# Performance work log

Hardware: AMD Instinct MI355X
Metric: run time of the kernel (lower is better)

## Reference

```python
import jax, jax.numpy as jnp
import numpy as np

B, N, DIM = 1, 512, 1024
HEADS, DH = 16, 64          # dim_head = 64, _dim = heads*dh = 1024
P = 32                      # projection_dim
P2 = P // 2
NEG_INF = -1e30


def setup_inputs() -> dict:
    key = jax.random.key(0)
    ks = jax.random.split(key, 14)
    s = 0.02
    _dim = HEADS * DH
    return {
        "x":    jax.random.normal(ks[0], (B, N, DIM), dtype=jnp.float32),
        "Wqkv": jax.random.normal(ks[1], (3 * _dim, DIM), dtype=jnp.float32) * s,
        "Wout": jax.random.normal(ks[2], (DIM, _dim), dtype=jnp.float32) * s,
        "Wq":   jax.random.normal(ks[3], (P, DH), dtype=jnp.float32) * s,
        "bq":   jax.random.normal(ks[4], (P,), dtype=jnp.float32) * s,
        "Wk":   jax.random.normal(ks[5], (P, DH), dtype=jnp.float32) * s,
        "bk":   jax.random.normal(ks[6], (P,), dtype=jnp.float32) * s,
        "W1":   jax.random.normal(ks[7], (P, 2 * P), dtype=jnp.float32) * s,
        "b1":   jax.random.normal(ks[8], (P,), dtype=jnp.float32) * s,
        "W2":   jax.random.normal(ks[9], (P2, P), dtype=jnp.float32) * s,
        "b2":   jax.random.normal(ks[10], (P2,), dtype=jnp.float32) * s,
        "W3":   jax.random.normal(ks[11], (1, P2), dtype=jnp.float32) * s,
        "b3":   jax.random.normal(ks[12], (1,), dtype=jnp.float32) * s,
    }


def reference(x, Wqkv, Wout, Wq, bq, Wk, bk, W1, b1, W2, b2, W3, b3):
    b, n, _ = x.shape
    # qkv projection, then einops 'b n (d k h) -> k b h n d' split (d outermost!)
    qkv = jnp.einsum('bnc,oc->bno', x, Wqkv).reshape(b, n, DH, 3, HEADS)
    q = jnp.transpose(qkv[:, :, :, 0, :], (0, 3, 1, 2))  # [b,h,n,dh]
    k = jnp.transpose(qkv[:, :, :, 1, :], (0, 3, 1, 2))
    v = jnp.transpose(qkv[:, :, :, 2, :], (0, 3, 1, 2))

    qp = jnp.einsum('bhnd,pd->bhnp', q, Wq) + bq  # [b,h,n,P]
    kp = jnp.einsum('bhnd,pd->bhnp', k, Wk) + bk

    # linear1 on concat(q_i, k_j): split W1 -> broadcast-add (same math,
    # avoids materializing the [b,h,n,n,2P] concat tensor)
    W1q, W1k = W1[:, :P], W1[:, P:]
    a = jnp.einsum('bhnp,qp->bhnq', qp, W1q)      # [b,h,n,P]
    c = jnp.einsum('bhnp,qp->bhnq', kp, W1k)      # [b,h,n,P]
    h1 = jax.nn.relu(a[:, :, :, None, :] + c[:, :, None, :, :] + b1)  # [b,h,n,n,P]
    h2 = jax.nn.relu(jnp.einsum('bhijp,qp->bhijq', h1, W2) + b2)      # [b,h,n,n,P/2]
    score = jnp.einsum('bhijq,oq->bhijo', h2, W3)[..., 0] + b3[0]     # [b,h,n,n]

    # causal mask (triu(1) filled with -inf)
    i = jnp.arange(n)
    causal = i[None, :] > i[:, None]
    score = jnp.where(causal, NEG_INF, score)

    attn = jax.nn.softmax(score, axis=-1)
    out = jnp.einsum('bhij,bhjd->bhid', attn, v)                      # [b,h,n,dh]
    out = jnp.transpose(out, (0, 2, 1, 3)).reshape(b, n, HEADS * DH)  # b n (h d)
    return jnp.einsum('bne,oe->bno', out, Wout)
```

## Files before the change

### kernel.cpp

```cpp
#include <hip/hip_runtime.h>
#include <hip/hip_bf16.h>
#include <hip/hip_fp16.h>
#include <math.h>

#define N_SEQ 512
#define DIM   1024
#define HEADS 16
#define DH    64
#define P     32
#define P2    16

typedef short    bf16x8 __attribute__((ext_vector_type(8)));
typedef _Float16 f16x8  __attribute__((ext_vector_type(8)));
typedef float    f32x4  __attribute__((ext_vector_type(4)));

__device__ inline unsigned short f2bf(float f) {
  union { float f; unsigned u; } v; v.f = f;
  unsigned r = (v.u + 0x7fffu + ((v.u >> 16) & 1u)) >> 16;
  return (unsigned short)r;
}

union H8 { f16x8 v; __half2 h2[4]; unsigned u32[4]; };

__global__ __launch_bounds__(256) void prep(
    const float* __restrict__ Wqkv, const float* __restrict__ Wq,
    const float* __restrict__ bq, const float* __restrict__ Wk,
    const float* __restrict__ bk, const float* __restrict__ W1,
    const float* __restrict__ x, const float* __restrict__ Wout,
    short* __restrict__ Wcomb, short* __restrict__ xb,
    short* __restrict__ Woutb, float* __restrict__ ba32,
    float* __restrict__ bc32) {
  const int b = blockIdx.x, tid = threadIdx.x;
  if (b < 256) {
    __shared__ float W1s[32][33];
    __shared__ float Wqs[32][65];
    __shared__ float wsm[32][65];
    __shared__ __align__(16) float qs[64][132];
    const int part = b >> 7, rem = b & 127;
    const int h = rem >> 3, c0 = (rem & 7) * 128;
    const int grow = part * 16 + h;
    for (int idx = tid; idx < 1024; idx += 256)
      W1s[idx >> 5][idx & 31] = W1[(idx >> 5) * 64 + part * 32 + (idx & 31)];
    const float* Wsel = part ? Wk : Wq;
    for (int idx = tid; idx < 2048; idx += 256)
      Wqs[idx >> 6][idx & 63] = Wsel[idx];
    for (int idx = tid; idx < 2048; idx += 256) {
      const int d = idx >> 5, c4 = idx & 31;
      *(float4*)&qs[d][c4 * 4] =
          *(const float4*)(Wqkv + (size_t)(d * 48 + grow) * DIM + c0 + c4 * 4);
    }
    __syncthreads();
    for (int idx = tid; idx < 2048; idx += 256) {
      const int q = idx >> 6, d = idx & 63;
      float s = 0.f;
#pragma unroll
      for (int p = 0; p < 32; ++p) s += W1s[q][p] * Wqs[p][d];
      wsm[q][d] = s;
    }
    __syncthreads();
    for (int idx = tid; idx < 4096; idx += 256) {
      const int q = idx >> 7, c = idx & 127;
      float s = 0.f;
#pragma unroll
      for (int d = 0; d < 64; ++d) s += wsm[q][d] * qs[d][c];
      Wcomb[(size_t)(part * 512 + h * 32 + q) * DIM + c0 + c] = (short)f2bf(s);
    }
    if (rem == 0 && tid < 32) {
      const float* bsel = part ? bk : bq;
      float s = 0.f;
#pragma unroll
      for (int p = 0; p < 32; ++p) s += W1s[tid][p] * bsel[p];
      (part ? bc32 : ba32)[tid] = s;
    }
  } else if (b < 384) {
#pragma unroll
    for (int rr = 0; rr < 8; ++rr) {
      const int ov = (b - 256) * 8 + rr;
      const int h = ov >> 6, d = ov & 63;
      const float4 v = *(const float4*)(Wqkv + (size_t)(d * 48 + 32 + h) * DIM + tid * 4);
      ushort4 o;
      o.x = f2bf(v.x); o.y = f2bf(v.y); o.z = f2bf(v.z); o.w = f2bf(v.w);
      *(ushort4*)(Wcomb + (size_t)(1024 + ov) * DIM + tid * 4) = o;
    }
  } else if (b < 512) {
    const int idx = (b - 384) * 256 + tid;
#pragma unroll
    for (int u = 0; u < 4; ++u) {
      const int t = u * 32768 + idx;
      const float4 v = ((const float4*)x)[t];
      ushort4 o;
      o.x = f2bf(v.x); o.y = f2bf(v.y); o.z = f2bf(v.z); o.w = f2bf(v.w);
      ((ushort4*)xb)[t] = o;
    }
  } else {
    const int idx = (b - 512) * 256 + tid;
#pragma unroll
    for (int u = 0; u < 4; ++u) {
      const int t = u * 65536 + idx;
      const float4 v = ((const float4*)Wout)[t];
      ushort4 o;
      o.x = f2bf(v.x); o.y = f2bf(v.y); o.z = f2bf(v.z); o.w = f2bf(v.w);
      ((ushort4*)Woutb)[t] = o;
    }
  }
}

__global__ __launch_bounds__(256) void gemm_acv(
    const short* __restrict__ xb, const short* __restrict__ Wcomb,
    const float* __restrict__ ba32, const float* __restrict__ bc32,
    const float* __restrict__ b1,
    __half* __restrict__ a_buf, __half* __restrict__ cb_buf,
    __half* __restrict__ vT) {
  const int wave = blockIdx.x * 4 + (threadIdx.x >> 6);
  const int tm = wave >> 6;
  const int tn = wave & 63;
  const int lane = threadIdx.x & 63;
  const int m = lane & 15;
  const int quad = lane >> 4;

  const short* pa  = xb + (size_t)(tm * 16 + m) * DIM + quad * 8;
  const short* pb0 = Wcomb + (size_t)(tn * 32 + m) * DIM + quad * 8;
  const short* pb1 = pb0 + (size_t)16 * DIM;

  f32x4 acc0 = {0.f,0.f,0.f,0.f}, acc1 = {0.f,0.f,0.f,0.f};
#pragma unroll 4
  for (int k = 0; k < DIM; k += 32) {
    const bf16x8 av = *(const bf16x8*)(pa + k);
    const bf16x8 b0 = *(const bf16x8*)(pb0 + k);
    const bf16x8 b1v = *(const bf16x8*)(pb1 + k);
    acc0 = __builtin_amdgcn_mfma_f32_16x16x32_bf16(av, b0, acc0, 0, 0, 0);
    acc1 = __builtin_amdgcn_mfma_f32_16x16x32_bf16(av, b1v, acc1, 0, 0, 0);
  }

#pragma unroll
  for (int r = 0; r < 4; ++r) {
    const int n = tm * 16 + quad * 4 + r;
#pragma unroll
    for (int half = 0; half < 2; ++half) {
      const int o = tn * 32 + m + half * 16;
      const float val = half ? acc1[r] : acc0[r];
      if (o < 512) {
        const int h = o >> 5, q = o & 31;
        a_buf[((size_t)h * N_SEQ + n) * P + q] = __float2half(val + ba32[q]);
      } else if (o < 1024) {
        const int oo = o - 512, h = oo >> 5, q = oo & 31;
        cb_buf[((size_t)h * N_SEQ + n) * P + q] = __float2half(val + bc32[q] + b1[q]);
      } else {
        const int ov = o - 1024, h = ov >> 6, d = ov & 63;
        vT[((size_t)h * DH + d) * N_SEQ + n] = __float2half(val);
      }
    }
  }
}

__device__ inline float rowscore(const H8& a, const H8& c, f16x8 w2f,
                                 float4 b2q, float4 w3q) {
  H8 u;
#pragma unroll
  for (int k = 0; k < 4; ++k) {
    const __half2 s = __hadd2(a.h2[k], c.h2[k]);
    union { __half2 h; unsigned u; } cv; cv.h = s;
    const unsigned msk = (cv.u >> 15) & 0x00010001u;
    u.u32[k] = cv.u & ~(msk * 0xFFFFu);
  }
  f32x4 acc = {0.f, 0.f, 0.f, 0.f};
  acc = __builtin_amdgcn_mfma_f32_16x16x32_f16(w2f, u.v, acc, 0, 0, 0);
  return fmaxf(acc[0] + b2q.x, 0.f) * w3q.x + fmaxf(acc[1] + b2q.y, 0.f) * w3q.y
       + fmaxf(acc[2] + b2q.z, 0.f) * w3q.z + fmaxf(acc[3] + b2q.w, 0.f) * w3q.w;
}

__global__ __launch_bounds__(64) void attn_score(
    const __half* __restrict__ a_g, const __half* __restrict__ cb_g,
    const float* __restrict__ W2, const float* __restrict__ b2,
    const float* __restrict__ W3, const float* __restrict__ b3,
    __half* __restrict__ prob) {
  const int it = blockIdx.x;
  const int h  = blockIdx.y;
  const int lane = threadIdx.x;
  const int m = lane & 15, quad = lane >> 4;

  __shared__ __align__(16) float sc[4][528];

  const int r0 = 2 * it, r1 = 2 * it + 1;
  const int r2 = 510 - 2 * it, r3 = 511 - 2 * it;
  const int n0 = (r0 >> 4) + 1, n1 = (r1 >> 4) + 1;
  const int n2 = (r2 >> 4) + 1, n3 = (r3 >> 4) + 1;
  const int ntq = (quad == 0) ? n0 : (quad == 1) ? n1 : (quad == 2) ? n2 : n3;

  f16x8 w2f;
  {
    const float4* wp = (const float4*)(W2 + m * P + quad * 8);
    const float4 w0 = wp[0], w1 = wp[1];
    H8 u;
    u.h2[0] = __floats2half2_rn(w0.x, w0.y);
    u.h2[1] = __floats2half2_rn(w0.z, w0.w);
    u.h2[2] = __floats2half2_rn(w1.x, w1.y);
    u.h2[3] = __floats2half2_rn(w1.z, w1.w);
    w2f = u.v;
  }
  const float4 b2q = *(const float4*)(b2 + quad * 4);
  const float4 w3q = *(const float4*)(W3 + quad * 4);
  const float b3v = b3[0];

  H8 a0, a1, a2, a3;
  a0.v = *(const f16x8*)(a_g + ((size_t)h * N_SEQ + r0) * P + quad * 8);
  a1.v = *(const f16x8*)(a_g + ((size_t)h * N_SEQ + r1) * P + quad * 8);
  a2.v = *(const f16x8*)(a_g + ((size_t)h * N_SEQ + r2) * P + quad * 8);
  a3.v = *(const f16x8*)(a_g + ((size_t)h * N_SEQ + r3) * P + quad * 8);

  float p0 = 0.f, p1 = 0.f, p2 = 0.f, p3 = 0.f;
  for (int jt = 0; jt < n3; ++jt) {
    H8 cb;
    cb.v = *(const f16x8*)(cb_g + ((size_t)h * N_SEQ + jt * 16 + m) * P + quad * 8);
    p3 = rowscore(a3, cb, w2f, b2q, w3q);
    if (jt < n2) p2 = rowscore(a2, cb, w2f, b2q, w3q);
    if (jt < n1) p1 = rowscore(a1, cb, w2f, b2q, w3q);
    if (jt < n0) p0 = rowscore(a0, cb, w2f, b2q, w3q);

    const float sx = (quad & 1) ? p0 : p1;
    const float sy = (quad & 1) ? p2 : p3;
    const float rx = __shfl_xor(sx, 16);
    const float ry = __shfl_xor(sy, 16);
    const float aa = ((quad & 1) ? p1 : p0) + rx;
    const float bb = ((quad & 1) ? p3 : p2) + ry;
    const float sz = (quad & 2) ? aa : bb;
    const float rz = __shfl_xor(sz, 32);
    const float fin = ((quad & 2) ? bb : aa) + rz;

    if (jt < ntq) sc[quad][jt * 16 + m] = fin + b3v;
  }
  __syncthreads();

  const int base = lane * 8;
#pragma unroll
  for (int r = 0; r < 4; ++r) {
    const int rq = (r == 0) ? r0 : (r == 1) ? r1 : (r == 2) ? r2 : r3;
    float v[8];
    *(float4*)&v[0] = *(const float4*)&sc[r][base];
    *(float4*)&v[4] = *(const float4*)&sc[r][base + 4];
    float mx = -1e30f;
#pragma unroll
    for (int u = 0; u < 8; ++u) if (base + u <= rq) mx = fmaxf(mx, v[u]);
#pragma unroll
    for (int msk = 1; msk < 64; msk <<= 1) mx = fmaxf(mx, __shfl_xor(mx, msk));
    float e[8], sum = 0.f;
#pragma unroll
    for (int u = 0; u < 8; ++u) {
      e[u] = (base + u <= rq) ? __expf(v[u] - mx) : 0.f;
      sum += e[u];
    }
#pragma unroll
    for (int msk = 1; msk < 64; msk <<= 1) sum += __shfl_xor(sum, msk);
    const float inv = 1.f / sum;
    H8 o;
    o.h2[0] = __floats2half2_rn(e[0] * inv, e[1] * inv);
    o.h2[1] = __floats2half2_rn(e[2] * inv, e[3] * inv);
    o.h2[2] = __floats2half2_rn(e[4] * inv, e[5] * inv);
    o.h2[3] = __floats2half2_rn(e[6] * inv, e[7] * inv);
    *(f16x8*)(prob + ((size_t)h * N_SEQ + rq) * N_SEQ + base) = o.v;
  }
}

__global__ __launch_bounds__(256) void attn_pv(
    const __half* __restrict__ prob, const __half* __restrict__ vT,
    short* __restrict__ attnb) {
  const int wave = blockIdx.x * 4 + (threadIdx.x >> 6);
  const int h = wave >> 7;
  const int rem = wave & 127;
  const int tm = rem >> 2;
  const int tn = rem & 3;
  const int lane = threadIdx.x & 63;
  const int m = lane & 15, quad = lane >> 4;

  const __half* pa = prob + ((size_t)h * N_SEQ + tm * 16 + m) * N_SEQ + quad * 8;
  const __half* pb = vT + ((size_t)h * DH + tn * 16 + m) * N_SEQ + quad * 8;

  f32x4 acc = {0.f, 0.f, 0.f, 0.f};
  const int kmax = tm * 16 + 16;
  for (int k = 0; k < kmax; k += 32) {
    const f16x8 a = *(const f16x8*)(pa + k);
    const f16x8 b = *(const f16x8*)(pb + k);
    acc = __builtin_amdgcn_mfma_f32_16x16x32_f16(a, b, acc, 0, 0, 0);
  }
#pragma unroll
  for (int r = 0; r < 4; ++r)
    attnb[(size_t)(tm * 16 + quad * 4 + r) * DIM + h * DH + tn * 16 + m] =
        (short)f2bf(acc[r]);
}

__global__ __launch_bounds__(256) void gemm_out16(
    const short* __restrict__ A, const short* __restrict__ B,
    float* __restrict__ C) {
  const int wave = blockIdx.x * 4 + (threadIdx.x >> 6);
  const int tm = wave >> 6;
  const int tn = wave & 63;
  const int lane = threadIdx.x & 63;
  const int m = lane & 15, quad = lane >> 4;

  const short* pa = A + (size_t)(tm * 16 + m) * DIM + quad * 8;
  const short* pb = B + (size_t)(tn * 16 + m) * DIM + quad * 8;

  f32x4 acc = {0.f, 0.f, 0.f, 0.f};
#pragma unroll 4
  for (int k = 0; k < DIM; k += 32) {
    const bf16x8 a = *(const bf16x8*)(pa + k);
    const bf16x8 b = *(const bf16x8*)(pb + k);
    acc = __builtin_amdgcn_mfma_f32_16x16x32_bf16(a, b, acc, 0, 0, 0);
  }
#pragma unroll
  for (int r = 0; r < 4; ++r)
    C[(size_t)(tm * 16 + quad * 4 + r) * DIM + tn * 16 + m] = acc[r];
}

extern "C" void kernel_launch(void* const* d_in, const int* in_sizes, int n_in,
                              void* d_out, int out_size, void* d_ws, size_t ws_size,
                              hipStream_t stream) {
  const float* x    = (const float*)d_in[0];
  const float* Wqkv = (const float*)d_in[1];
  const float* Wout = (const float*)d_in[2];
  const float* Wq   = (const float*)d_in[3];
  const float* bq   = (const float*)d_in[4];
  const float* Wk   = (const float*)d_in[5];
  const float* bk   = (const float*)d_in[6];
  const float* W1   = (const float*)d_in[7];
  const float* b1   = (const float*)d_in[8];
  const float* W2   = (const float*)d_in[9];
  const float* b2   = (const float*)d_in[10];
  const float* W3   = (const float*)d_in[11];
  const float* b3   = (const float*)d_in[12];
  float* out = (float*)d_out;

  float*  ws     = (float*)d_ws;
  float*  ba32   = ws;
  float*  bc32   = ba32 + 32;
  __half* a_buf  = (__half*)(bc32 + 32);
  __half* cb_buf = a_buf + (size_t)HEADS * N_SEQ * P;
  __half* vT     = cb_buf + (size_t)HEADS * N_SEQ * P;
  __half* prob   = vT + (size_t)HEADS * DH * N_SEQ;
  short*  Wcomb  = (short*)(prob + (size_t)HEADS * N_SEQ * N_SEQ);
  short*  xb     = Wcomb + (size_t)2048 * DIM;
  short*  Woutb  = xb + (size_t)N_SEQ * DIM;
  short*  attnb  = Woutb + (size_t)DIM * DIM;

  prep<<<768, 256, 0, stream>>>(Wqkv, Wq, bq, Wk, bk, W1, x, Wout,
                                Wcomb, xb, Woutb, ba32, bc32);

  gemm_acv<<<512, 256, 0, stream>>>(xb, Wcomb, ba32, bc32, b1,
                                    a_buf, cb_buf, vT);

  dim3 g3(128, HEADS);
  attn_score<<<g3, 64, 0, stream>>>(a_buf, cb_buf, W2, b2, W3, b3, prob);

  attn_pv<<<512, 256, 0, stream>>>(prob, vT, attnb);

  gemm_out16<<<512, 256, 0, stream>>>(attnb, Woutb, out);
}
```

Before: 178.0 us.

## Fuse pairwise score, softmax and PV into one attention kernel

Merges the score/softmax kernel and the P·V kernel into one kernel that keeps a 32-row probability tile in shared memory as fp16. This removes the global round trip of the [16,512,512] prob matrix and one launch. It also drops b3 because softmax is shift-invariant, and applies the 1/sum normalization after the PV MFMA. The grid shrinks from 2048 single-wave blocks to 256 four-wave blocks. Raw scores stored in fp16 before softmax may reduce precision, and the lower block count may underuse the GPU.

```diff
diff --git a/kernel.cpp b/kernel.cpp
--- a/kernel.cpp
+++ b/kernel.cpp
@@ -9,6 +9,7 @@
 #define DH    64
 #define P     32
 #define P2    16
+#define PSTR  520
 
 typedef short    bf16x8 __attribute__((ext_vector_type(8)));
 typedef _Float16 f16x8  __attribute__((ext_vector_type(8)));
@@ -169,123 +170,145 @@
        + fmaxf(acc[2] + b2q.z, 0.f) * w3q.z + fmaxf(acc[3] + b2q.w, 0.f) * w3q.w;
 }
 
-__global__ __launch_bounds__(64) void attn_score(
+__device__ inline float quadreduce4(float p0, float p1, float p2, float p3,
+                                    int quad) {
+  const float sx = (quad & 1) ? p0 : p1;
+  const float sy = (quad & 1) ? p2 : p3;
+  const float rx = __shfl_xor(sx, 16);
+  const float ry = __shfl_xor(sy, 16);
+  const float aa = ((quad & 1) ? p1 : p0) + rx;
+  const float bb = ((quad & 1) ? p3 : p2) + ry;
+  const float sz = (quad & 2) ? aa : bb;
+  const float rz = __shfl_xor(sz, 32);
+  return ((quad & 2) ? bb : aa) + rz;
+}
+
+__global__ __launch_bounds__(256) void attn_fused(
     const __half* __restrict__ a_g, const __half* __restrict__ cb_g,
     const float* __restrict__ W2, const float* __restrict__ b2,
-    const float* __restrict__ W3, const float* __restrict__ b3,
-    __half* __restrict__ prob) {
-  const int it = blockIdx.x;
-  const int h  = blockIdx.y;
-  const int lane = threadIdx.x;
+    const float* __restrict__ W3,
+    const __half* __restrict__ vT, short* __restrict__ attnb) {
+  const int p = blockIdx.x;
+  const int h = blockIdx.y;
+  const int tid = threadIdx.x;
+  const int w = tid >> 6;
+  const int lane = tid & 63;
   const int m = lane & 15, quad = lane >> 4;
 
-  __shared__ __align__(16) float sc[4][528];
-
-  const int r0 = 2 * it, r1 = 2 * it + 1;
-  const int r2 = 510 - 2 * it, r3 = 511 - 2 * it;
-  const int n0 = (r0 >> 4) + 1, n1 = (r1 >> 4) + 1;
-  const int n2 = (r2 >> 4) + 1, n3 = (r3 >> 4) + 1;
-  const int ntq = (quad == 0) ? n0 : (quad == 1) ? n1 : (quad == 2) ? n2 : n3;
-
-  f16x8 w2f;
+  __shared__ __align__(16) __half probS[32][PSTR];
+  __shared__ float invS[32];
+
+  const int tlo = p, thi = 31 - p;
+  const int nlo = p + 1, nhi = 32 - p;
+
   {
-    const float4* wp = (const float4*)(W2 + m * P + quad * 8);
-    const float4 w0 = wp[0], w1 = wp[1];
-    H8 u;
-    u.h2[0] = __floats2half2_rn(w0.x, w0.y);
-    u.h2[1] = __floats2half2_rn(w0.z, w0.w);
-    u.h2[2] = __floats2half2_rn(w1.x, w1.y);
-    u.h2[3] = __floats2half2_rn(w1.z, w1.w);
-    w2f = u.v;
-  }
-  const float4 b2q = *(const float4*)(b2 + quad * 4);
-  const float4 w3q = *(const float4*)(W3 + quad * 4);
-  const float b3v = b3[0];
-
-  H8 a0, a1, a2, a3;
-  a0.v = *(const f16x8*)(a_g + ((size_t)h * N_SEQ + r0) * P + quad * 8);
-  a1.v = *(const f16x8*)(a_g + ((size_t)h * N_SEQ + r1) * P + quad * 8);
-  a2.v = *(const f16x8*)(a_g + ((size_t)h * N_SEQ + r2) * P + quad * 8);
-  a3.v = *(const f16x8*)(a_g + ((size_t)h * N_SEQ + r3) * P + quad * 8);
-
-  float p0 = 0.f, p1 = 0.f, p2 = 0.f, p3 = 0.f;
-  for (int jt = 0; jt < n3; ++jt) {
-    H8 cb;
-    cb.v = *(const f16x8*)(cb_g + ((size_t)h * N_SEQ + jt * 16 + m) * P + quad * 8);
-    p3 = rowscore(a3, cb, w2f, b2q, w3q);
-    if (jt < n2) p2 = rowscore(a2, cb, w2f, b2q, w3q);
-    if (jt < n1) p1 = rowscore(a1, cb, w2f, b2q, w3q);
-    if (jt < n0) p0 = rowscore(a0, cb, w2f, b2q, w3q);
-
-    const float sx = (quad & 1) ? p0 : p1;
-    const float sy = (quad & 1) ? p2 : p3;
-    const float rx = __shfl_xor(sx, 16);
-    const float ry = __shfl_xor(sy, 16);
-    const float aa = ((quad & 1) ? p1 : p0) + rx;
-    const float bb = ((quad & 1) ? p3 : p2) + ry;
-    const float sz = (quad & 2) ? aa : bb;
-    const float rz = __shfl_xor(sz, 32);
-    const float fin = ((quad & 2) ? bb : aa) + rz;
-
-    if (jt < ntq) sc[quad][jt * 16 + m] = fin + b3v;
+    f16x8 w2f;
+    {
+      const float4* wp = (const float4*)(W2 + m * P + quad * 8);
+      const float4 w0 = wp[0], w1 = wp[1];
+      H8 u;
+      u.h2[0] = __floats2half2_rn(w0.x, w0.y);
+      u.h2[1] = __floats2half2_rn(w0.z, w0.w);
+      u.h2[2] = __floats2half2_rn(w1.x, w1.y);
+      u.h2[3] = __floats2half2_rn(w1.z, w1.w);
+      w2f = u.v;
+    }
+    const float4 b2q = *(const float4*)(b2 + quad * 4);
+    const float4 w3q = *(const float4*)(W3 + quad * 4);
+
+    H8 alo[4], ahi[4];
+#pragma unroll
+    for (int r = 0; r < 4; ++r) {
+      alo[r].v = *(const f16x8*)(a_g + ((size_t)h * N_SEQ + tlo * 16 + 4 * w + r) * P + quad * 8);
+      ahi[r].v = *(const f16x8*)(a_g + ((size_t)h * N_SEQ + thi * 16 + 4 * w + r) * P + quad * 8);
+    }
+
+    for (int jt = 0; jt < nhi; ++jt) {
+      H8 cb;
+      cb.v = *(const f16x8*)(cb_g + ((size_t)h * N_SEQ + jt * 16 + m) * P + quad * 8);
+      const float q0 = rowscore(ahi[0], cb, w2f, b2q, w3q);
+      const float q1 = rowscore(ahi[1], cb, w2f, b2q, w3q);
+      const float q2 = rowscore(ahi[2], cb, w2f, b2q, w3q);
+      const float q3 = rowscore(ahi[3], cb, w2f, b2q, w3q);
+      const float fh = quadreduce4(q0, q1, q2, q3, quad);
+      probS[16 + 4 * w + quad][jt * 16 + m] = __float2half(fh);
+      if (jt < nlo) {
+        const float s0 = rowscore(alo[0], cb, w2f, b2q, w3q);
+        const float s1 = rowscore(alo[1], cb, w2f, b2q, w3q);
+        const float s2 = rowscore(alo[2], cb, w2f, b2q, w3q);
+        const float s3 = rowscore(alo[3], cb, w2f, b2q, w3q);
+        const float fl = quadreduce4(s0, s1, s2, s3, quad);
+        probS[4 * w + quad][jt * 16 + m] = __float2half(fl);
+      }
+    }
   }
   __syncthreads();
 
-  const int base = lane * 8;
-#pragma unroll
-  for (int r = 0; r < 4; ++r) {
-    const int rq = (r == 0) ? r0 : (r == 1) ? r1 : (r == 2) ? r2 : r3;
-    float v[8];
-    *(float4*)&v[0] = *(const float4*)&sc[r][base];
-    *(float4*)&v[4] = *(const float4*)&sc[r][base + 4];
+  {
+    const int lr = 8 * w + (lane >> 3);
+    const int c  = lane & 7;
+    const int gi = (lr < 16) ? (tlo * 16 + lr) : (thi * 16 + (lr - 16));
     float mx = -1e30f;
 #pragma unroll
-    for (int u = 0; u < 8; ++u) if (base + u <= rq) mx = fmaxf(mx, v[u]);
-#pragma unroll
-    for (int msk = 1; msk < 64; msk <<= 1) mx = fmaxf(mx, __shfl_xor(mx, msk));
-    float e[8], sum = 0.f;
-#pragma unroll
-    for (int u = 0; u < 8; ++u) {
-      e[u] = (base + u <= rq) ? __expf(v[u] - mx) : 0.f;
-      sum += e[u];
-    }
-#pragma unroll
-    for (int msk = 1; msk < 64; msk <<= 1) sum += __shfl_xor(sum, msk);
-    const float inv = 1.f / sum;
-    H8 o;
-    o.h2[0] = __floats2half2_rn(e[0] * inv, e[1] * inv);
-    o.h2[1] = __floats2half2_rn(e[2] * inv, e[3] * inv);
-    o.h2[2] = __floats2half2_rn(e[4] * inv, e[5] * inv);
-    o.h2[3] = __floats2half2_rn(e[6] * inv, e[7] * inv);
-    *(f16x8*)(prob + ((size_t)h * N_SEQ + rq) * N_SEQ + base) = o.v;
-  }
-}
-
-__global__ __launch_bounds__(256) void attn_pv(
-    const __half* __restrict__ prob, const __half* __restrict__ vT,
-    short* __restrict__ attnb) {
-  const int wave = blockIdx.x * 4 + (threadIdx.x >> 6);
-  const int h = wave >> 7;
-  const int rem = wave & 127;
-  const int tm = rem >> 2;
-  const int tn = rem & 3;
-  const int lane = threadIdx.x & 63;
-  const int m = lane & 15, quad = lane >> 4;
-
-  const __half* pa = prob + ((size_t)h * N_SEQ + tm * 16 + m) * N_SEQ + quad * 8;
-  const __half* pb = vT + ((size_t)h * DH + tn * 16 + m) * N_SEQ + quad * 8;
-
-  f32x4 acc = {0.f, 0.f, 0.f, 0.f};
-  const int kmax = tm * 16 + 16;
-  for (int k = 0; k < kmax; k += 32) {
-    const f16x8 a = *(const f16x8*)(pa + k);
-    const f16x8 b = *(const f16x8*)(pb + k);
-    acc = __builtin_amdgcn_mfma_f32_16x16x32_f16(a, b, acc, 0, 0, 0);
-  }
-#pragma unroll
-  for (int r = 0; r < 4; ++r)
-    attnb[(size_t)(tm * 16 + quad * 4 + r) * DIM + h * DH + tn * 16 + m] =
-        (short)f2bf(acc[r]);
+    for (int k = 0; k < 8; ++k) {
+      const int c0 = k * 64 + c * 8;
+      if (c0 > gi) break;
+      H8 vv; vv.v = *(const f16x8*)&probS[lr][c0];
+#pragma unroll
+      for (int u = 0; u < 8; ++u) {
+        const float s = __half2float(vv.h2[u >> 1].data[u & 1]);
+        if (c0 + u <= gi) mx = fmaxf(mx, s);
+      }
+    }
+#pragma unroll
+    for (int msk = 1; msk < 8; msk <<= 1) mx = fmaxf(mx, __shfl_xor(mx, msk));
+    float sum = 0.f;
+#pragma unroll
+    for (int k = 0; k < 8; ++k) {
+      const int c0 = k * 64 + c * 8;
+      H8 vv; vv.v = *(const f16x8*)&probS[lr][c0];
+      H8 o;
+#pragma unroll
+      for (int u = 0; u < 4; ++u) {
+        float e0 = 0.f, e1 = 0.f;
+        if (c0 + 2 * u <= gi) {
+          e0 = __expf(__half2float(vv.h2[u].data[0]) - mx);
+          if (c0 + 2 * u + 1 <= gi)
+            e1 = __expf(__half2float(vv.h2[u].data[1]) - mx);
+        }
+        sum += e0 + e1;
+        o.h2[u] = __floats2half2_rn(e0, e1);
+      }
+      *(f16x8*)&probS[lr][c0] = o.v;
+    }
+#pragma unroll
+    for (int msk = 1; msk < 8; msk <<= 1) sum += __shfl_xor(sum, msk);
+    if (c == 0) invS[lr] = 1.f / sum;
+  }
+  __syncthreads();
+
+  {
+    const int d0 = w * 16;
+    const __half* pb = vT + ((size_t)h * DH + d0 + m) * N_SEQ + quad * 8;
+#pragma unroll
+    for (int half = 0; half < 2; ++half) {
+      const int lbase = half ? 16 : 0;
+      const int tile = half ? thi : tlo;
+      const int nk = half ? ((33 - p) >> 1) : ((p + 2) >> 1);
+      f32x4 acc = {0.f, 0.f, 0.f, 0.f};
+      for (int k = 0; k < nk; ++k) {
+        const f16x8 a = *(const f16x8*)&probS[lbase + m][k * 32 + quad * 8];
+        const f16x8 b = *(const f16x8*)(pb + k * 32);
+        acc = __builtin_amdgcn_mfma_f32_16x16x32_f16(a, b, acc, 0, 0, 0);
+      }
+#pragma unroll
+      for (int r = 0; r < 4; ++r) {
+        const int lrow = quad * 4 + r;
+        const float val = acc[r] * invS[lbase + lrow];
+        attnb[(size_t)(tile * 16 + lrow) * DIM + h * DH + d0 + m] = (short)f2bf(val);
+      }
+    }
+  }
 }
 
 __global__ __launch_bounds__(256) void gemm_out16(
@@ -327,7 +350,6 @@
   const float* W2   = (const float*)d_in[9];
   const float* b2   = (const float*)d_in[10];
   const float* W3   = (const float*)d_in[11];
-  const float* b3   = (const float*)d_in[12];
   float* out = (float*)d_out;
 
   float*  ws     = (float*)d_ws;
@@ -336,8 +358,7 @@
   __half* a_buf  = (__half*)(bc32 + 32);
   __half* cb_buf = a_buf + (size_t)HEADS * N_SEQ * P;
   __half* vT     = cb_buf + (size_t)HEADS * N_SEQ * P;
-  __half* prob   = vT + (size_t)HEADS * DH * N_SEQ;
-  short*  Wcomb  = (short*)(prob + (size_t)HEADS * N_SEQ * N_SEQ);
+  short*  Wcomb  = (short*)(vT + (size_t)HEADS * DH * N_SEQ);
   short*  xb     = Wcomb + (size_t)2048 * DIM;
   short*  Woutb  = xb + (size_t)N_SEQ * DIM;
   short*  attnb  = Woutb + (size_t)DIM * DIM;
@@ -348,10 +369,8 @@
   gemm_acv<<<512, 256, 0, stream>>>(xb, Wcomb, ba32, bc32, b1,
                                     a_buf, cb_buf, vT);
 
-  dim3 g3(128, HEADS);
-  attn_score<<<g3, 64, 0, stream>>>(a_buf, cb_buf, W2, b2, W3, b3, prob);
-
-  attn_pv<<<512, 256, 0, stream>>>(prob, vT, attnb);
+  dim3 g3(16, HEADS);
+  attn_fused<<<g3, 256, 0, stream>>>(a_buf, cb_buf, W2, b2, W3, vT, attnb);
 
   gemm_out16<<<512, 256, 0, stream>>>(attnb, Woutb, out);
 }
```

Measured after the change: 174.1 us. 1.02x faster.
